# Optimization experiments

Measured on AMD Instinct MI355X. Metric: run time of the kernel, lower is better.

## Reference

```python
import jax, jax.numpy as jnp
import numpy as np
from jax import lax

N_QUBITS = 10
N_LAYERS = 6
DIM = 1 << N_QUBITS
EPS = 1e-5

_i = np.arange(DIM)
# Z_SIGNS[w, i] = (+1/-1) eigenvalue of PauliZ on wire w (wire 0 = most significant bit)
Z_SIGNS = jnp.asarray(np.stack([1.0 - 2.0 * ((_i >> (N_QUBITS - 1 - w)) & 1) for w in range(N_QUBITS)]).astype(np.float32))

def _layer_perm(r):
    # composed permutation of the ring of CNOT(w, (w+r)%n) gates of one StronglyEntanglingLayers layer
    p = _i.copy()
    for w in range(N_QUBITS):
        c, t = w, (w + r) % N_QUBITS
        pc, pt = N_QUBITS - 1 - c, N_QUBITS - 1 - t
        pg = _i ^ (((_i >> pc) & 1) << pt)
        p = p[pg]
    return p

LAYER_PERMS = [jnp.asarray(_layer_perm(l % (N_QUBITS - 1) + 1), dtype=jnp.int32) for l in range(N_LAYERS)]

def _apply_1q(state, U, wire):
    # state: (B, DIM) complex64; U: (2,2) or batched (B,2,2)
    B = state.shape[0]
    left = 1 << wire
    right = DIM // (2 * left)
    s = state.reshape(B, left, 2, right)
    if U.ndim == 3:
        out = jnp.einsum('bij,bljr->blir', U, s)
    else:
        out = jnp.einsum('ij,bljr->blir', U, s)
    return out.reshape(B, DIM)

def _ry_batched(theta):
    c = jnp.cos(theta / 2)
    s = jnp.sin(theta / 2)
    return jnp.stack([jnp.stack([c, -s], -1), jnp.stack([s, c], -1)], -2).astype(jnp.complex64)

def _rot(phi, theta, omega):
    # PennyLane Rot(phi, theta, omega) = RZ(omega) @ RY(theta) @ RZ(phi)
    c = jnp.cos(theta / 2)
    s = jnp.sin(theta / 2)
    m00 = jnp.exp(-1j * (phi + omega) / 2) * c
    m01 = -jnp.exp(1j * (phi - omega) / 2) * s
    m10 = jnp.exp(-1j * (phi - omega) / 2) * s
    m11 = jnp.exp(1j * (phi + omega) / 2) * c
    return jnp.stack([jnp.stack([m00, m01]), jnp.stack([m10, m11])]).astype(jnp.complex64)

def quantum_forward(xq, qw):
    # batched statevector simulation of: RY(pi*x_i) encoding + StronglyEntanglingLayers
    B = xq.shape[0]
    state = jnp.zeros((B, DIM), jnp.complex64).at[:, 0].set(1.0)
    for w in range(N_QUBITS):
        state = _apply_1q(state, _ry_batched(jnp.pi * xq[:, w]), w)
    for l in range(N_LAYERS):
        for w in range(N_QUBITS):
            state = _apply_1q(state, _rot(qw[l, w, 0], qw[l, w, 1], qw[l, w, 2]), w)
        state = state[:, LAYER_PERMS[l]]
    probs = state.real ** 2 + state.imag ** 2
    return probs @ Z_SIGNS.T  # (B, N_QUBITS) expvals of PauliZ

def _conv(x, w, b):
    y = lax.conv_general_dilated(x, w, (1, 1), 'SAME', dimension_numbers=('NCHW', 'OIHW', 'NCHW'))
    return y + b[None, :, None, None]

def _bn(x, g, b):
    # BatchNorm2d in training mode: per-batch statistics over (N, H, W)
    m = jnp.mean(x, (0, 2, 3), keepdims=True)
    v = jnp.var(x, (0, 2, 3), keepdims=True)
    return (x - m) * lax.rsqrt(v + EPS) * g[None, :, None, None] + b[None, :, None, None]

def _pool(x):
    return lax.reduce_window(x, -jnp.inf, lax.max, (1, 1, 2, 2), (1, 1, 2, 2), 'VALID')

def setup_inputs() -> dict:
    key = jax.random.key(0)
    ks = jax.random.split(key, 16)
    n = lambda k, sh, sc: jax.random.normal(k, sh, jnp.float32) * sc
    return {
        'x': jax.random.normal(ks[0], (256, 3, 64, 64), jnp.float32),
        'conv1_w': n(ks[1], (32, 3, 3, 3), 0.1), 'conv1_b': jnp.zeros(32),
        'bn1_g': jnp.ones(32), 'bn1_b': jnp.zeros(32),
        'conv2_w': n(ks[2], (32, 32, 3, 3), 0.05), 'conv2_b': jnp.zeros(32),
        'bn2_g': jnp.ones(32), 'bn2_b': jnp.zeros(32),
        'conv3_w': n(ks[3], (64, 32, 3, 3), 0.05), 'conv3_b': jnp.zeros(64),
        'bn3_g': jnp.ones(64), 'bn3_b': jnp.zeros(64),
        'conv4_w': n(ks[4], (64, 64, 3, 3), 0.05), 'conv4_b': jnp.zeros(64),
        'bn4_g': jnp.ones(64), 'bn4_b': jnp.zeros(64),
        'fc1_w': n(ks[5], (128, 64 * 16 * 16), 0.01), 'fc1_b': jnp.zeros(128),
        'fc2_w': n(ks[6], (10, 128), 0.05), 'fc2_b': jnp.zeros(10),
        'q_weights': jax.random.uniform(ks[7], (6, 10, 3), jnp.float32),
        'head_w': n(ks[8], (10, 10), 0.1), 'head_b': jnp.zeros(10),
    }

def reference(x, conv1_w, conv1_b, bn1_g, bn1_b, conv2_w, conv2_b, bn2_g, bn2_b,
              conv3_w, conv3_b, bn3_g, bn3_b, conv4_w, conv4_b, bn4_g, bn4_b,
              fc1_w, fc1_b, fc2_w, fc2_b, q_weights, head_w, head_b):
    h = jax.nn.relu(_bn(_conv(x, conv1_w, conv1_b), bn1_g, bn1_b))
    h = jax.nn.relu(_bn(_conv(h, conv2_w, conv2_b), bn2_g, bn2_b))
    h = _pool(h)  # Dropout(0.25) is identity in eval
    h = jax.nn.relu(_bn(_conv(h, conv3_w, conv3_b), bn3_g, bn3_b))
    h = jax.nn.relu(_bn(_conv(h, conv4_w, conv4_b), bn4_g, bn4_b))
    h = _pool(h)
    h = h.reshape(h.shape[0], -1)  # (B, 64*16*16)
    h = jax.nn.relu(h @ fc1_w.T + fc1_b)
    h = h @ fc2_w.T + fc2_b  # (B, n_qubits)
    q = quantum_forward(h, q_weights)
    return q @ head_w.T + head_b  # (B, num_classes)
```

## Files before the change

### kernel.cpp

```cpp
#include <hip/hip_runtime.h>
#include <math.h>

#define PI_F 3.14159265358979323846f

typedef __attribute__((ext_vector_type(8))) _Float16 half8;
typedef __attribute__((ext_vector_type(4))) _Float16 half4;
typedef __attribute__((ext_vector_type(4))) float f32x4;

__global__ __launch_bounds__(256) void prep_kernel(
    const float* __restrict__ x, _Float16* __restrict__ X4P,
    const float* __restrict__ w1, const float* __restrict__ w2,
    const float* __restrict__ w3, const float* __restrict__ w4,
    _Float16* __restrict__ t1, _Float16* __restrict__ t2,
    _Float16* __restrict__ t3, _Float16* __restrict__ t4,
    const float* __restrict__ f1w, _Float16* __restrict__ w1t,
    const float* __restrict__ qw, float* __restrict__ rotm,
    unsigned short* __restrict__ perm)
{
    const int b = blockIdx.x;
    const int t = threadIdx.x;
    if (b < 2380) {
        int pp = (b * 256 + t) * 2;
        half8 o;
        #pragma unroll
        for (int j = 0; j < 2; ++j) {
            int p = pp + j;
            int n = p / 4760;
            int rem = p - n * 4760;
            int yp = rem / 68, xp = rem - (rem / 68) * 68;
            int gy = yp - 2, gx = xp - 2;
            float v0 = 0.f, v1 = 0.f, v2 = 0.f;
            if (gy >= 0 && gy < 64 && gx >= 0 && gx < 64) {
                const float* xb = x + (size_t)n * 12288 + gy * 64 + gx;
                v0 = xb[0]; v1 = xb[4096]; v2 = xb[8192];
            }
            o[j * 4 + 0] = (_Float16)v0;
            o[j * 4 + 1] = (_Float16)v1;
            o[j * 4 + 2] = (_Float16)v2;
            o[j * 4 + 3] = (_Float16)0.f;
        }
        *(half8*)&X4P[(size_t)pp * 4] = o;
    } else if (b < 2640) {
        int idx = (b - 2380) * 256 + t;
        if (idx < 9216) {
            int j = idx & 7, co = (idx >> 3) & 31, k8 = idx >> 8;
            int k = k8 * 8 + j, tap = k >> 5, ci = k & 31;
            t2[idx] = (_Float16)w2[(size_t)(co * 32 + ci) * 9 + tap];
        } else if (idx < 27648) {
            int e = idx - 9216;
            int j = e & 7, co = (e >> 3) & 31, r = e >> 8;
            int k8 = r % 36, gg = r / 36;
            int k = k8 * 8 + j, tap = k >> 5, ci = k & 31;
            t3[e] = (_Float16)w3[(size_t)((gg * 32 + co) * 32 + ci) * 9 + tap];
        } else if (idx < 64512) {
            int e = idx - 27648;
            int j = e & 7, co = (e >> 3) & 31, r = e >> 8;
            int k8 = r % 36, gc = r / 36;
            int g = gc >> 1, cc = gc & 1;
            int kl = k8 * 8 + j, tap = kl >> 5, ci = cc * 32 + (kl & 31);
            t4[e] = (_Float16)w4[(size_t)((g * 32 + co) * 64 + ci) * 9 + tap];
        } else if (idx < 66560) {
            int e = idx - 64512;
            int j = e & 7, co = (e >> 3) & 31, k8 = e >> 8;
            int k = k8 * 8 + j, tap = k >> 2, ci = k & 3;
            t1[e] = (_Float16)((tap < 9 && ci < 3) ? w1[(size_t)(co * 3 + ci) * 9 + tap] : 0.f);
        }
    } else if (b < 3152) {
        __shared__ float lds[64][65];
        int b2 = b - 2640;
        const int yx0 = (b2 & 3) * 64;
        const int j = b2 >> 2;
        #pragma unroll
        for (int i = 0; i < 16; ++i) {
            int idx = t + 256 * i;
            int c = idx >> 6, yxl = idx & 63;
            lds[c][yxl] = f1w[(size_t)j * 16384 + c * 256 + yx0 + yxl];
        }
        __syncthreads();
        #pragma unroll
        for (int i = 0; i < 2; ++i) {
            int idx = t + 256 * i;
            int yxl = idx >> 3, c8 = idx & 7;
            half8 h;
            #pragma unroll
            for (int jj = 0; jj < 8; ++jj)
                h[jj] = (_Float16)lds[c8 * 8 + jj][yxl];
            *(half8*)&w1t[(size_t)j * 16384 + (size_t)(yx0 + yxl) * 64 + c8 * 8] = h;
        }
    } else {
        if (t < 60) {
            float phi = qw[t * 3], th = qw[t * 3 + 1], om = qw[t * 3 + 2];
            float c = cosf(0.5f * th), s = sinf(0.5f * th);
            float apo = 0.5f * (phi + om), amo = 0.5f * (phi - om);
            float cpo = cosf(apo), spo = sinf(apo);
            float cmo = cosf(amo), smo = sinf(amo);
            rotm[t * 8 + 0] = cpo * c;  rotm[t * 8 + 1] = -spo * c;
            rotm[t * 8 + 2] = -cmo * s; rotm[t * 8 + 3] = -smo * s;
            rotm[t * 8 + 4] = cmo * s;  rotm[t * 8 + 5] = -smo * s;
            rotm[t * 8 + 6] = cpo * c;  rotm[t * 8 + 7] = spo * c;
        }
        for (int e = t; e < 6144; e += 256) {
            int layer = e >> 10, i = e & 1023;
            int r = layer % 9 + 1;
            int jdx = i;
            for (int w = 9; w >= 0; --w) {
                int tt = (w + r) % 10;
                int pc = 9 - w, pt_ = 9 - tt;
                jdx ^= ((jdx >> pc) & 1) << pt_;
            }
            perm[e] = (unsigned short)jdx;
        }
    }
}

__global__ __launch_bounds__(256) void conv1_stats_kernel(
    const _Float16* __restrict__ X4P, const _Float16* __restrict__ w1m,
    const float* __restrict__ bias, _Float16* __restrict__ Yg,
    float* __restrict__ partials)
{
    constexpr int TC = 66, TR = 6;
    constexpr int NPIX = (TR + 1) * TC;
    __shared__ __align__(16) _Float16 s_in[NPIX * 4];
    __shared__ __align__(16) _Float16 s_w[2048];
    __shared__ __align__(16) _Float16 s_y[256 * 32];
    __shared__ float s_red[64];

    const int t = threadIdx.x;
    const int row0 = blockIdx.x * 4;
    const int n = blockIdx.z;

    *(half8*)&s_w[t * 8] = *(const half8*)&w1m[t * 8];

    for (int p = t; p < NPIX; p += 256) {
        int col = p % TC, r = p / TC;
        uint2 u = make_uint2(0u, 0u);
        if (r < TR) {
            size_t pb = ((size_t)(n * 70 + row0 + r + 1) * 68 + col + 1) * 4;
            u = *(const uint2*)&X4P[pb];
        }
        *(uint2*)&s_in[p * 4] = u;
    }
    if (t < 64) s_red[t] = 0.f;
    __syncthreads();

    const int w = t >> 6, l = t & 63;
    const int lm = l & 15, lg = l >> 4;
    int pA[4];
    #pragma unroll
    for (int f = 0; f < 4; ++f) {
        int m = w * 64 + f * 16 + lm;
        pA[f] = (m >> 6) * TC + (m & 63);
    }
    f32x4 zero4 = {0.f, 0.f, 0.f, 0.f};
    f32x4 acc[4][2];
    #pragma unroll
    for (int f = 0; f < 4; ++f) { acc[f][0] = zero4; acc[f][1] = zero4; }

    {
        const int t0 = lg * 2;
        const int off0 = (t0 / 3) * TC + (t0 % 3);
        const int off1 = ((t0 + 1) / 3) * TC + ((t0 + 1) % 3);
        half8 b0 = *(const half8*)&s_w[(lg * 32 + lm) * 8];
        half8 b1 = *(const half8*)&s_w[(lg * 32 + 16 + lm) * 8];
        #pragma unroll
        for (int f = 0; f < 4; ++f) {
            half4 alo = *(const half4*)&s_in[(pA[f] + off0) * 4];
            half4 ahi = *(const half4*)&s_in[(pA[f] + off1) * 4];
            half8 a;
            #pragma unroll
            for (int j = 0; j < 4; ++j) { a[j] = alo[j]; a[4 + j] = ahi[j]; }
            acc[f][0] = __builtin_amdgcn_mfma_f32_16x16x32_f16(a, b0, acc[f][0], 0, 0, 0);
            acc[f][1] = __builtin_amdgcn_mfma_f32_16x16x32_f16(a, b1, acc[f][1], 0, 0, 0);
        }
    }
    {
        half8 b0 = *(const half8*)&s_w[((4 + lg) * 32 + lm) * 8];
        half8 b1 = *(const half8*)&s_w[((4 + lg) * 32 + 16 + lm) * 8];
        #pragma unroll
        for (int f = 0; f < 4; ++f) {
            half8 a;
            #pragma unroll
            for (int j = 0; j < 8; ++j) a[j] = (_Float16)0.f;
            if (lg == 0) {
                half4 alo = *(const half4*)&s_in[(pA[f] + 134) * 4];
                half4 ahi = *(const half4*)&s_in[(pA[f] + 198) * 4];
                #pragma unroll
                for (int j = 0; j < 4; ++j) { a[j] = alo[j]; a[4 + j] = ahi[j]; }
            }
            acc[f][0] = __builtin_amdgcn_mfma_f32_16x16x32_f16(a, b0, acc[f][0], 0, 0, 0);
            acc[f][1] = __builtin_amdgcn_mfma_f32_16x16x32_f16(a, b1, acc[f][1], 0, 0, 0);
        }
    }

    float bv0 = bias[lm];
    float bv1 = bias[16 + lm];
    float s0 = 0.f, s20 = 0.f, s1 = 0.f, s21 = 0.f;
    #pragma unroll
    for (int f = 0; f < 4; ++f) {
        #pragma unroll
        for (int r = 0; r < 4; ++r) {
            float v0 = acc[f][0][r] + bv0;
            float v1 = acc[f][1][r] + bv1;
            int p_loc = w * 64 + f * 16 + lg * 4 + r;
            s_y[p_loc * 32 + lm] = (_Float16)v0;
            s_y[p_loc * 32 + 16 + lm] = (_Float16)v1;
            s0 += v0; s20 += v0 * v0;
            s1 += v1; s21 += v1 * v1;
        }
    }
    s0 += __shfl_xor(s0, 16);  s0 += __shfl_xor(s0, 32);
    s1 += __shfl_xor(s1, 16);  s1 += __shfl_xor(s1, 32);
    s20 += __shfl_xor(s20, 16); s20 += __shfl_xor(s20, 32);
    s21 += __shfl_xor(s21, 16); s21 += __shfl_xor(s21, 32);
    if (l < 16) {
        atomicAdd(&s_red[lm], s0);
        atomicAdd(&s_red[16 + lm], s1);
        atomicAdd(&s_red[32 + lm], s20);
        atomicAdd(&s_red[48 + lm], s21);
    }
    __syncthreads();

    {
        _Float16* Yb = Yg + ((size_t)(n * 64 + row0) * 64) * 32;
        #pragma unroll
        for (int i = 0; i < 4; ++i) {
            int idx = t + 256 * i;
            *(half8*)&Yb[(size_t)idx * 8] = *(const half8*)&s_y[idx * 8];
        }
    }
    if (t < 64)
        partials[((size_t)n * 16 + blockIdx.x) * 64 + t] = s_red[t];
}

__global__ __launch_bounds__(512, 6) void conv2_fused_kernel(
    const _Float16* __restrict__ Yg, const _Float16* __restrict__ ssh1,
    const _Float16* __restrict__ wt2, const float* __restrict__ c2bias,
    _Float16* __restrict__ out0, _Float16* __restrict__ out1,
    float* __restrict__ partials)
{
    constexpr int COUT = 32, MF = 4, NB = 2;
    constexpr int ROWS = 8;
    constexpr int TC = 66, NPIX = 10 * 66;
    constexpr int PS = 36;
    __shared__ __align__(16) _Float16 s_in[NPIX * PS];
    __shared__ float s_red[64];

    const int t = threadIdx.x;
    const int row0 = blockIdx.x * ROWS;
    const int n = blockIdx.z;
    const int w = t >> 6, l = t & 63;
    const int lm = l & 15, lg = l >> 4;

    if (t < 64) s_red[t] = 0.f;

    {
        const int c8 = t & 3;
        half8 sc = *(const half8*)&ssh1[c8 * 8];
        half8 sh = *(const half8*)&ssh1[32 + c8 * 8];
        for (int idx = t; idx < NPIX * 4; idx += 512) {
            int p = idx >> 2;
            int py = p / 66, px = p - py * 66;
            int gy = row0 - 1 + py, gx = px - 1;
            half8 v;
            #pragma unroll
            for (int j = 0; j < 8; ++j) v[j] = (_Float16)0.f;
            if (gy >= 0 && gy < 64 && gx >= 0 && gx < 64) {
                half8 y = *(const half8*)&Yg[(((size_t)n * 64 + gy) * 64 + gx) * 32 + c8 * 8];
                #pragma unroll
                for (int j = 0; j < 8; ++j) {
                    _Float16 f = y[j] * sc[j] + sh[j];
                    v[j] = f > (_Float16)0.f ? f : (_Float16)0.f;
                }
            }
            half4* vp = (half4*)&v;
            *(half4*)&s_in[p * PS + c8 * 8] = vp[0];
            *(half4*)&s_in[p * PS + c8 * 8 + 4] = vp[1];
        }
    }
    __syncthreads();

    int pA[MF];
    #pragma unroll
    for (int f = 0; f < MF; ++f)
        pA[f] = w * TC + f * 16 + lm;
    f32x4 zero4 = {0.f, 0.f, 0.f, 0.f};
    f32x4 acc[MF][NB];
    #pragma unroll
    for (int f = 0; f < MF; ++f)
        #pragma unroll
        for (int nb = 0; nb < NB; ++nb) acc[f][nb] = zero4;

    #pragma unroll
    for (int tap = 0; tap < 9; ++tap) {
        const int dy = tap / 3, dx = tap % 3;
        const int poff = dy * TC + dx;
        half8 b[NB];
        #pragma unroll
        for (int nb = 0; nb < NB; ++nb) {
            int col = nb * 16 + lm;
            b[nb] = *(const half8*)&wt2[((tap * 4 + lg) * 32 + col) * 8];
        }
        #pragma unroll
        for (int f = 0; f < MF; ++f) {
            int p = pA[f] + poff;
            half4 alo = *(const half4*)&s_in[p * PS + lg * 8];
            half4 ahi = *(const half4*)&s_in[p * PS + lg * 8 + 4];
            half8 a;
            #pragma unroll
            for (int j = 0; j < 4; ++j) { a[j] = alo[j]; a[4 + j] = ahi[j]; }
            #pragma unroll
            for (int nb = 0; nb < NB; ++nb)
                acc[f][nb] = __builtin_amdgcn_mfma_f32_16x16x32_f16(a, b[nb], acc[f][nb], 0, 0, 0);
        }
    }

    float bv[NB], s[NB], s2[NB];
    #pragma unroll
    for (int nb = 0; nb < NB; ++nb) {
        bv[nb] = c2bias[nb * 16 + lm];
        s[nb] = 0.f; s2[nb] = 0.f;
    }
    #pragma unroll
    for (int f = 0; f < MF; ++f) {
        #pragma unroll
        for (int nb = 0; nb < NB; ++nb) {
            #pragma unroll
            for (int r = 0; r < 4; ++r) {
                float v = acc[f][nb][r] + bv[nb];
                acc[f][nb][r] = v;
                s[nb] += v; s2[nb] += v * v;
            }
        }
    }
    #pragma unroll
    for (int nb = 0; nb < NB; ++nb) {
        s[nb] += __shfl_xor(s[nb], 16);  s[nb] += __shfl_xor(s[nb], 32);
        s2[nb] += __shfl_xor(s2[nb], 16); s2[nb] += __shfl_xor(s2[nb], 32);
    }
    if (l < 16) {
        #pragma unroll
        for (int nb = 0; nb < NB; ++nb) {
            atomicAdd(&s_red[nb * 16 + lm], s[nb]);
            atomicAdd(&s_red[32 + nb * 16 + lm], s2[nb]);
        }
    }

    {
        __syncthreads();
        _Float16* pk = s_in;
        #pragma unroll
        for (int nb = 0; nb < NB; ++nb) {
            #pragma unroll
            for (int f = 0; f < MF; ++f) {
                float v0 = acc[f][nb][0], v1 = acc[f][nb][1];
                float v2 = acc[f][nb][2], v3 = acc[f][nb][3];
                int xp0 = f * 8 + lg * 2;
                int o0 = (w * 32 + xp0) * COUT + nb * 16 + lm;
                int o1 = (w * 32 + xp0 + 1) * COUT + nb * 16 + lm;
                pk[o0] = (_Float16)fminf(v0, v1);
                pk[8192 + o0] = (_Float16)fmaxf(v0, v1);
                pk[o1] = (_Float16)fminf(v2, v3);
                pk[8192 + o1] = (_Float16)fmaxf(v2, v3);
            }
        }
        __syncthreads();
        int hp_row = t >> 7, rem = t & 127;
        int xp = rem >> 2, c8 = rem & 3;
        half8 mnA = *(const half8*)&pk[((2 * hp_row) * 32 + xp) * COUT + c8 * 8];
        half8 mnB = *(const half8*)&pk[((2 * hp_row + 1) * 32 + xp) * COUT + c8 * 8];
        half8 mxA = *(const half8*)&pk[8192 + ((2 * hp_row) * 32 + xp) * COUT + c8 * 8];
        half8 mxB = *(const half8*)&pk[8192 + ((2 * hp_row + 1) * 32 + xp) * COUT + c8 * 8];
        half8 mn, mx;
        #pragma unroll
        for (int j = 0; j < 8; ++j) {
            mn[j] = mnA[j] < mnB[j] ? mnA[j] : mnB[j];
            mx[j] = mxA[j] > mxB[j] ? mxA[j] : mxB[j];
        }
        size_t ob = (((size_t)n * 32 + (row0 >> 1) + hp_row) * 32 + xp) * COUT + c8 * 8;
        *(half8*)&out0[ob] = mn;
        *(half8*)&out1[ob] = mx;
    }

    __syncthreads();
    if (t < 64) {
        size_t bid = (size_t)n * gridDim.x + blockIdx.x;
        partials[bid * 64 + t] = s_red[t];
    }
}

template<int BLOCK, int W, int CIN, int COUT, int MF, int NB,
         bool MMIN, bool POOL>
__global__ __launch_bounds__(BLOCK, (BLOCK == 512 ? 4 : 3)) void conv_mfma_kernel(
    const _Float16* __restrict__ in0, const _Float16* __restrict__ in1,
    const _Float16* __restrict__ coef, const _Float16* __restrict__ wt,
    const float* __restrict__ bias,
    _Float16* __restrict__ out0, _Float16* __restrict__ out1,
    float* __restrict__ partials)
{
    constexpr int H = W;
    constexpr int NWAVE = BLOCK / 64;
    constexpr int SPW = MF * 16;
    constexpr int ROWS = NWAVE * SPW / W;
    constexpr int TR = ROWS + 2;
    constexpr int TC = W + 2;
    constexpr int NPIX = TR * TC;
    constexpr int NCH = CIN / 32;
    constexpr int C8N = CIN / 8;
    constexpr int KC = 288;
    constexpr int COUTB = NB * 16;
    __shared__ __align__(16) _Float16 s_in[NPIX * CIN];
    __shared__ float s_red[2 * COUTB];

    const int t = threadIdx.x;
    const int row0 = blockIdx.x * ROWS;
    const int n = blockIdx.z;

    const int w = t >> 6, l = t & 63;
    const int lm = l & 15, lg = l >> 4;
    int pA[MF];
    #pragma unroll
    for (int f = 0; f < MF; ++f) {
        int m = w * SPW + f * 16 + lm;
        pA[f] = (m / W) * TC + (m % W);
    }
    f32x4 zero4 = {0.f, 0.f, 0.f, 0.f};
    f32x4 acc[MF][NB];
    #pragma unroll
    for (int f = 0; f < MF; ++f)
        #pragma unroll
        for (int nb = 0; nb < NB; ++nb) acc[f][nb] = zero4;
    if (t < 2 * COUTB) s_red[t] = 0.f;

    for (int idx = t; idx < NPIX * C8N; idx += BLOCK) {
        int c8 = idx % C8N;
        int p = idx / C8N;
        int col = p % TC, r = p / TC;
        int gy = row0 + r - 1, gx = col - 1;
        half8 v;
        #pragma unroll
        for (int j = 0; j < 8; ++j) v[j] = (_Float16)0.f;
        if (gy >= 0 && gy < H && gx >= 0 && gx < W) {
            size_t gidx = (((size_t)n * H + gy) * W + gx) * CIN + c8 * 8;
            if (MMIN) {
                half8 mn = *(const half8*)&in0[gidx];
                half8 mx = *(const half8*)&in1[gidx];
                half8 sa = *(const half8*)&coef[c8 * 8];
                half8 sb = *(const half8*)&coef[CIN + c8 * 8];
                half8 sh = *(const half8*)&coef[2 * CIN + c8 * 8];
                #pragma unroll
                for (int j = 0; j < 8; ++j) {
                    _Float16 f = mx[j] * sa[j] + mn[j] * sb[j] + sh[j];
                    v[j] = f > (_Float16)0.f ? f : (_Float16)0.f;
                }
            } else {
                v = *(const half8*)&in0[gidx];
                if (coef) {
                    half8 sc = *(const half8*)&coef[c8 * 8];
                    half8 sh = *(const half8*)&coef[CIN + c8 * 8];
                    #pragma unroll
                    for (int j = 0; j < 8; ++j) {
                        _Float16 f = v[j] * sc[j] + sh[j];
                        v[j] = f > (_Float16)0.f ? f : (_Float16)0.f;
                    }
                }
            }
        }
        *(half8*)&s_in[(c8 * NPIX + p) * 8] = v;
    }
    __syncthreads();

    #pragma unroll
    for (int tap = 0; tap < 9; ++tap) {
        const int dy = tap / 3, dx = tap % 3;
        const int poff = dy * TC + dx;
        #pragma unroll
        for (int cc = 0; cc < NCH; ++cc) {
            half8 b[NB];
            #pragma unroll
            for (int nb = 0; nb < NB; ++nb) {
                int cog = nb * 16 + lm;
                int gg = cog >> 5, col = cog & 31;
                const _Float16* wp = wt + (size_t)(gg * NCH + cc) * KC * 32;
                b[nb] = *(const half8*)&wp[((tap * 4 + lg) * 32 + col) * 8];
            }
            #pragma unroll
            for (int f = 0; f < MF; ++f) {
                half8 a = *(const half8*)&s_in[((cc * 4 + lg) * NPIX + pA[f] + poff) * 8];
                #pragma unroll
                for (int nb = 0; nb < NB; ++nb)
                    acc[f][nb] = __builtin_amdgcn_mfma_f32_16x16x32_f16(a, b[nb], acc[f][nb], 0, 0, 0);
            }
        }
    }

    float bv[NB], s[NB], s2[NB];
    #pragma unroll
    for (int nb = 0; nb < NB; ++nb) {
        bv[nb] = bias[nb * 16 + lm];
        s[nb] = 0.f; s2[nb] = 0.f;
    }
    #pragma unroll
    for (int f = 0; f < MF; ++f) {
        #pragma unroll
        for (int r = 0; r < 4; ++r) {
            int m = w * SPW + f * 16 + lg * 4 + r;
            int yy = row0 + m / W, xo = m % W;
            size_t base = (((size_t)n * H + yy) * W + xo) * COUT;
            #pragma unroll
            for (int nb = 0; nb < NB; ++nb) {
                float v = acc[f][nb][r] + bv[nb];
                if (!POOL) out0[base + nb * 16 + lm] = (_Float16)v;
                s[nb] += v; s2[nb] += v * v;
            }
        }
    }
    #pragma unroll
    for (int nb = 0; nb < NB; ++nb) {
        s[nb] += __shfl_xor(s[nb], 16);  s[nb] += __shfl_xor(s[nb], 32);
        s2[nb] += __shfl_xor(s2[nb], 16); s2[nb] += __shfl_xor(s2[nb], 32);
    }
    if (l < 16) {
        #pragma unroll
        for (int nb = 0; nb < NB; ++nb) {
            atomicAdd(&s_red[nb * 16 + lm], s[nb]);
            atomicAdd(&s_red[COUTB + nb * 16 + lm], s2[nb]);
        }
    }

    if (POOL) {
        constexpr int FH = MF / 2;
        constexpr int PPIX = (ROWS / 2) * (W / 2);
        static_assert(2 * PPIX * COUT <= NPIX * CIN, "pool pack fits in s_in");
        __syncthreads();
        _Float16* pk = s_in;
        #pragma unroll
        for (int nb = 0; nb < NB; ++nb) {
            #pragma unroll
            for (int f = 0; f < FH; ++f) {
                #pragma unroll
                for (int rp = 0; rp < 2; ++rp) {
                    float a0 = acc[f][nb][2 * rp] + bv[nb];
                    float a1 = acc[f][nb][2 * rp + 1] + bv[nb];
                    float a2 = acc[f + FH][nb][2 * rp] + bv[nb];
                    float a3 = acc[f + FH][nb][2 * rp + 1] + bv[nb];
                    float mn = fminf(fminf(a0, a1), fminf(a2, a3));
                    float mx = fmaxf(fmaxf(a0, a1), fmaxf(a2, a3));
                    int xp = f * 8 + lg * 2 + rp;
                    int o = (w * (W / 2) + xp) * COUT + nb * 16 + lm;
                    pk[o] = (_Float16)mn;
                    pk[PPIX * COUT + o] = (_Float16)mx;
                }
            }
        }
        __syncthreads();
        size_t gb = (((size_t)n * (H / 2) + (row0 >> 1)) * (W / 2)) * COUT;
        for (int idx = t; idx < PPIX * COUT / 8; idx += BLOCK) {
            *(half8*)&out0[gb + (size_t)idx * 8] = *(const half8*)&pk[idx * 8];
            *(half8*)&out1[gb + (size_t)idx * 8] = *(const half8*)&pk[(PPIX * COUT + idx * 8)];
        }
    }

    __syncthreads();
    if (t < 2 * COUTB) {
        size_t bid = (size_t)n * gridDim.x + blockIdx.x;
        partials[bid * 2 * COUTB + t] = s_red[t];
    }
}

__global__ __launch_bounds__(256) void bn_finalize_kernel(
    const float* __restrict__ partials, int nx, float inv_count,
    const float* __restrict__ gamma, const float* __restrict__ beta,
    float* __restrict__ ss, _Float16* __restrict__ ssh,
    _Float16* __restrict__ sab, int COUT)
{
    const int c = blockIdx.x;
    const int t = threadIdx.x;
    float sum = 0.f, sq = 0.f;
    int total = 256 * nx;
    for (int e = t; e < total; e += 256) {
        size_t off = (size_t)e * 2 * COUT;
        sum += partials[off + c];
        sq  += partials[off + COUT + c];
    }
    #pragma unroll
    for (int off = 32; off > 0; off >>= 1) {
        sum += __shfl_xor(sum, off);
        sq  += __shfl_xor(sq, off);
    }
    __shared__ float rs[4], rq[4];
    if ((t & 63) == 0) { rs[t >> 6] = sum; rq[t >> 6] = sq; }
    __syncthreads();
    if (t == 0) {
        sum = rs[0] + rs[1] + rs[2] + rs[3];
        sq  = rq[0] + rq[1] + rq[2] + rq[3];
        float mean = sum * inv_count;
        float var = sq * inv_count - mean * mean;
        float scale = gamma[c] * rsqrtf(var + 1e-5f);
        float shift = beta[c] - mean * scale;
        ss[c] = scale;
        ss[COUT + c] = shift;
        if (ssh) {
            ssh[c] = (_Float16)scale;
            ssh[COUT + c] = (_Float16)shift;
        }
        if (sab) {
            sab[c] = (_Float16)(scale > 0.f ? scale : 0.f);
            sab[COUT + c] = (_Float16)(scale > 0.f ? 0.f : scale);
            sab[2 * COUT + c] = (_Float16)shift;
        }
    }
}

__global__ __launch_bounds__(256) void fc1_mfma_kernel(
    const _Float16* __restrict__ Amin, const _Float16* __restrict__ Amax,
    const _Float16* __restrict__ sab, const _Float16* __restrict__ Bw,
    float* __restrict__ hp)
{
    __shared__ __align__(16) _Float16 As[64][72];
    __shared__ __align__(16) _Float16 Bs[128][72];
    const int t = threadIdx.x;
    const int mt = blockIdx.x;
    const int kc = blockIdx.y;
    const int w = t >> 6, l = t & 63;
    const int lm = l & 15, lg = l >> 4;

    f32x4 zero4 = {0.f, 0.f, 0.f, 0.f};
    f32x4 acc[8];
    #pragma unroll
    for (int nb = 0; nb < 8; ++nb) acc[nb] = zero4;

    const size_t a_base = (size_t)(mt * 64) * 16384 + (size_t)kc * 512;
    const size_t b_base = (size_t)kc * 512;

    for (int p = 0; p < 8; ++p) {
        __syncthreads();
        #pragma unroll
        for (int i = 0; i < 2; ++i) {
            int idx = t + 256 * i;
            int r = idx >> 3, c8 = idx & 7;
            size_t off = a_base + (size_t)r * 16384 + p * 64 + c8 * 8;
            half8 mn = *(const half8*)&Amin[off];
            half8 mx = *(const half8*)&Amax[off];
            half8 sa = *(const half8*)&sab[c8 * 8];
            half8 sb = *(const half8*)&sab[64 + c8 * 8];
            half8 sh = *(const half8*)&sab[128 + c8 * 8];
            half8 v;
            #pragma unroll
            for (int j = 0; j < 8; ++j) {
                _Float16 f = mx[j] * sa[j] + mn[j] * sb[j] + sh[j];
                v[j] = f > (_Float16)0.f ? f : (_Float16)0.f;
            }
            *(half8*)&As[r][c8 * 8] = v;
        }
        #pragma unroll
        for (int i = 0; i < 4; ++i) {
            int idx = t + 256 * i;
            int r = idx >> 3, c8 = idx & 7;
            *(half8*)&Bs[r][c8 * 8] =
                *(const half8*)&Bw[b_base + (size_t)r * 16384 + p * 64 + c8 * 8];
        }
        __syncthreads();
        #pragma unroll
        for (int ks = 0; ks < 64; ks += 32) {
            half8 a = *(const half8*)&As[w * 16 + lm][ks + lg * 8];
            #pragma unroll
            for (int nb = 0; nb < 8; ++nb) {
                half8 b = *(const half8*)&Bs[nb * 16 + lm][ks + lg * 8];
                acc[nb] = __builtin_amdgcn_mfma_f32_16x16x32_f16(a, b, acc[nb], 0, 0, 0);
            }
        }
    }
    #pragma unroll
    for (int nb = 0; nb < 8; ++nb) {
        #pragma unroll
        for (int r = 0; r < 4; ++r) {
            int row = mt * 64 + w * 16 + lg * 4 + r;
            hp[((size_t)kc * 256 + row) * 128 + nb * 16 + lm] = acc[nb][r];
        }
    }
}

__global__ __launch_bounds__(128) void fcq_kernel(
    const float* __restrict__ hp, const float* __restrict__ f1b,
    const float* __restrict__ f2w, const float* __restrict__ f2b,
    const float* __restrict__ rotm, const unsigned short* __restrict__ perm,
    const float* __restrict__ head_w, const float* __restrict__ head_b,
    float* __restrict__ outp)
{
    __shared__ float lds[2048];
    __shared__ float hl[128];
    __shared__ float xql[10];
    const int n = blockIdx.x;
    const int t = threadIdx.x;

    {
        float s = f1b[t];
        #pragma unroll
        for (int kc = 0; kc < 32; ++kc) s += hp[((size_t)kc * 256 + n) * 128 + t];
        hl[t] = fmaxf(0.f, s);
    }
    __syncthreads();
    if (t < 10) {
        float o = f2b[t];
        #pragma unroll 4
        for (int k = 0; k < 128; ++k) o += f2w[t * 128 + k] * hl[k];
        xql[t] = o;
    }
    __syncthreads();
    if (t >= 64) return;

    const int l = t;
    float ar[16], ai[16];
    #pragma unroll
    for (int r = 0; r < 16; ++r) { ar[r] = 0.f; ai[r] = 0.f; }
    if (l == 0) ar[0] = 1.f;

    #pragma unroll
    for (int w = 0; w < 10; ++w) {
        float th = 0.5f * PI_F * xql[w];
        float c = cosf(th), s = sinf(th);
        const int k = 9 - w;
        if (k >= 6) {
            const int b = k - 6;
            #pragma unroll
            for (int r = 0; r < 16; ++r) {
                if (!(r & (1 << b))) {
                    int r1 = r | (1 << b);
                    float a0 = ar[r], a1 = ar[r1];
                    ar[r]  = c * a0 - s * a1;
                    ar[r1] = s * a0 + c * a1;
                }
            }
        } else {
            float ss = ((l >> k) & 1) ? s : -s;
            #pragma unroll
            for (int r = 0; r < 16; ++r) {
                float p = __shfl_xor(ar[r], 1 << k);
                ar[r] = c * ar[r] + ss * p;
            }
        }
    }

    #pragma unroll 1
    for (int layer = 0; layer < 6; ++layer) {
        #pragma unroll
        for (int w = 0; w < 10; ++w) {
            const float* m = rotm + (layer * 10 + w) * 8;
            float m00r = m[0], m00i = m[1], m01r = m[2], m01i = m[3];
            float m10r = m[4], m10i = m[5], m11r = m[6], m11i = m[7];
            const int k = 9 - w;
            if (k >= 6) {
                const int b = k - 6;
                #pragma unroll
                for (int r = 0; r < 16; ++r) {
                    if (!(r & (1 << b))) {
                        int r1 = r | (1 << b);
                        float a0r = ar[r], a0i = ai[r];
                        float a1r = ar[r1], a1i = ai[r1];
                        ar[r]  = m00r * a0r - m00i * a0i + m01r * a1r - m01i * a1i;
                        ai[r]  = m00r * a0i + m00i * a0r + m01r * a1i + m01i * a1r;
                        ar[r1] = m10r * a0r - m10i * a0i + m11r * a1r - m11i * a1i;
                        ai[r1] = m10r * a0i + m10i * a0r + m11r * a1i + m11i * a1r;
                    }
                }
            } else {
                int bit = (l >> k) & 1;
                float mAr = bit ? m11r : m00r, mAi = bit ? m11i : m00i;
                float mBr = bit ? m10r : m01r, mBi = bit ? m10i : m01i;
                #pragma unroll
                for (int r = 0; r < 16; ++r) {
                    float pr = __shfl_xor(ar[r], 1 << k);
                    float pi = __shfl_xor(ai[r], 1 << k);
                    float mr = ar[r], mi = ai[r];
                    ar[r] = mAr * mr - mAi * mi + mBr * pr - mBi * pi;
                    ai[r] = mAr * mi + mAi * mr + mBr * pi + mBi * pr;
                }
            }
        }
        #pragma unroll
        for (int r = 0; r < 16; ++r) {
            lds[(r << 6) | l] = ar[r];
            lds[1024 + ((r << 6) | l)] = ai[r];
        }
        __syncthreads();
        const unsigned short* pt = perm + layer * 1024;
        #pragma unroll
        for (int r = 0; r < 16; ++r) {
            int ji = pt[(r << 6) | l];
            ar[r] = lds[ji];
            ai[r] = lds[1024 + ji];
        }
        __syncthreads();
    }

    float S = 0.f, T0 = 0.f, T1 = 0.f, T2 = 0.f, T3 = 0.f;
    #pragma unroll
    for (int r = 0; r < 16; ++r) {
        float pr = ar[r] * ar[r] + ai[r] * ai[r];
        S += pr;
        T0 += (r & 1) ? -pr : pr;
        T1 += (r & 2) ? -pr : pr;
        T2 += (r & 4) ? -pr : pr;
        T3 += (r & 8) ? -pr : pr;
    }
    float pk[10];
    pk[0] = T3; pk[1] = T2; pk[2] = T1; pk[3] = T0;
    #pragma unroll
    for (int w = 4; w < 10; ++w)
        pk[w] = ((l >> (9 - w)) & 1) ? -S : S;
    #pragma unroll
    for (int w = 0; w < 10; ++w) {
        #pragma unroll
        for (int off = 1; off < 64; off <<= 1)
            pk[w] += __shfl_xor(pk[w], off);
    }
    if (l < 10) {
        float o = head_b[l];
        #pragma unroll
        for (int kk = 0; kk < 10; ++kk) o += pk[kk] * head_w[l * 10 + kk];
        outp[n * 10 + l] = o;
    }
}

extern "C" void kernel_launch(void* const* d_in, const int* in_sizes, int n_in,
                              void* d_out, int out_size, void* d_ws, size_t ws_size,
                              hipStream_t stream)
{
    const float* x   = (const float*)d_in[0];
    const float* c1w = (const float*)d_in[1];  const float* c1b = (const float*)d_in[2];
    const float* g1  = (const float*)d_in[3];  const float* b1  = (const float*)d_in[4];
    const float* c2w = (const float*)d_in[5];  const float* c2b = (const float*)d_in[6];
    const float* g2  = (const float*)d_in[7];  const float* b2  = (const float*)d_in[8];
    const float* c3w = (const float*)d_in[9];  const float* c3b = (const float*)d_in[10];
    const float* g3  = (const float*)d_in[11]; const float* b3  = (const float*)d_in[12];
    const float* c4w = (const float*)d_in[13]; const float* c4b = (const float*)d_in[14];
    const float* g4  = (const float*)d_in[15]; const float* b4  = (const float*)d_in[16];
    const float* f1w = (const float*)d_in[17]; const float* f1b = (const float*)d_in[18];
    const float* f2w = (const float*)d_in[19]; const float* f2b = (const float*)d_in[20];
    const float* qw  = (const float*)d_in[21];
    const float* hw  = (const float*)d_in[22]; const float* hb  = (const float*)d_in[23];

    float* ws = (float*)d_ws;
    _Float16* H0 = (_Float16*)ws;
    _Float16* H1 = H0 + 33554432;
    float* part = ws + 33554432;
    float* ss1  = part + 524288;
    float* ss2  = ss1 + 64;
    float* ss3  = ss2 + 64;
    float* ss4  = ss3 + 128;
    float* hp   = ss4 + 128;
    float* rotm = hp + 1048576;
    unsigned short* perm16 = (unsigned short*)(rotm + 480);
    _Float16* ssh1 = (_Float16*)(perm16 + 6144);
    _Float16* ssh3 = ssh1 + 64;
    _Float16* sab2 = ssh3 + 128;
    _Float16* sab4 = sab2 + 96;
    _Float16* wt2  = sab4 + 192;
    _Float16* wt3  = wt2 + 9216;
    _Float16* wt4  = wt3 + 18432;
    _Float16* w1m  = wt4 + 36864;
    _Float16* w1t  = w1m + 2048;
    _Float16* X4P  = w1t + 2097152;

    _Float16* Yg    = H0;
    _Float16* minT2 = H1;
    _Float16* maxT2 = H1 + 8388608;
    _Float16* minT4 = H1;
    _Float16* maxT4 = H1 + 4194304;

    prep_kernel<<<3153, 256, 0, stream>>>(x, X4P, c1w, c2w, c3w, c4w,
                                          w1m, wt2, wt3, wt4, f1w, w1t,
                                          qw, rotm, perm16);

    conv1_stats_kernel<<<dim3(16, 1, 256), 256, 0, stream>>>(
        X4P, w1m, c1b, Yg, part);
    bn_finalize_kernel<<<32, 256, 0, stream>>>(part, 16, 1.f / 1048576.f,
                                               g1, b1, ss1, ssh1, nullptr, 32);

    conv2_fused_kernel<<<dim3(8, 1, 256), 512, 0, stream>>>(
        Yg, ssh1, wt2, c2b, minT2, maxT2, part);
    bn_finalize_kernel<<<32, 256, 0, stream>>>(part, 8, 1.f / 1048576.f,
                                               g2, b2, ss2, nullptr, sab2, 32);

    conv_mfma_kernel<512, 32, 32, 64, 4, 4, true, false>
        <<<dim3(2, 1, 256), 512, 0, stream>>>(
        minT2, maxT2, sab2, wt3, c3b, H0, nullptr, part);
    bn_finalize_kernel<<<64, 256, 0, stream>>>(part, 2, 1.f / 262144.f,
                                               g3, b3, ss3, ssh3, nullptr, 64);

    conv_mfma_kernel<512, 32, 64, 64, 4, 4, false, true>
        <<<dim3(2, 1, 256), 512, 0, stream>>>(
        H0, nullptr, ssh3, wt4, c4b, minT4, maxT4, part);
    bn_finalize_kernel<<<64, 256, 0, stream>>>(part, 2, 1.f / 262144.f,
                                               g4, b4, ss4, nullptr, sab4, 64);

    fc1_mfma_kernel<<<dim3(4, 32), 256, 0, stream>>>(minT4, maxT4, sab4, w1t, hp);

    fcq_kernel<<<256, 128, 0, stream>>>(hp, f1b, f2w, f2b,
                                        rotm, perm16, hw, hb, (float*)d_out);
}
```

Measured before the change: 194.9 us.

## Split quantum statevector simulation across four waves with LDS exchange for high qubits

```diff
diff --git a/kernel.cpp b/kernel.cpp
--- a/kernel.cpp
+++ b/kernel.cpp
@@ -680,20 +680,23 @@
     }
 }
 
-__global__ __launch_bounds__(128) void fcq_kernel(
+__global__ __launch_bounds__(256) void fcq_kernel(
     const float* __restrict__ hp, const float* __restrict__ f1b,
     const float* __restrict__ f2w, const float* __restrict__ f2b,
     const float* __restrict__ rotm, const unsigned short* __restrict__ perm,
     const float* __restrict__ head_w, const float* __restrict__ head_b,
     float* __restrict__ outp)
 {
-    __shared__ float lds[2048];
+    __shared__ float lre[1024];
+    __shared__ float lim[1024];
     __shared__ float hl[128];
     __shared__ float xql[10];
     const int n = blockIdx.x;
     const int t = threadIdx.x;
-
-    {
+    const int l = t & 63;
+    const int wv = t >> 6;
+
+    if (t < 128) {
         float s = f1b[t];
         #pragma unroll
         for (int kc = 0; kc < 32; ++kc) s += hp[((size_t)kc * 256 + n) * 128 + t];
@@ -707,23 +710,22 @@
         xql[t] = o;
     }
     __syncthreads();
-    if (t >= 64) return;
-
-    const int l = t;
-    float ar[16], ai[16];
-    #pragma unroll
-    for (int r = 0; r < 16; ++r) { ar[r] = 0.f; ai[r] = 0.f; }
-    if (l == 0) ar[0] = 1.f;
+
+    const int ampb = (wv << 6) | l;
+    float ar[4], ai[4];
+    #pragma unroll
+    for (int r = 0; r < 4; ++r) { ar[r] = 0.f; ai[r] = 0.f; }
+    if (t == 0) ar[0] = 1.f;
 
     #pragma unroll
     for (int w = 0; w < 10; ++w) {
         float th = 0.5f * PI_F * xql[w];
         float c = cosf(th), s = sinf(th);
         const int k = 9 - w;
-        if (k >= 6) {
-            const int b = k - 6;
-            #pragma unroll
-            for (int r = 0; r < 16; ++r) {
+        if (k >= 8) {
+            const int b = k - 8;
+            #pragma unroll
+            for (int r = 0; r < 4; ++r) {
                 if (!(r & (1 << b))) {
                     int r1 = r | (1 << b);
                     float a0 = ar[r], a1 = ar[r1];
@@ -731,10 +733,21 @@
                     ar[r1] = s * a0 + c * a1;
                 }
             }
+        } else if (k >= 6) {
+            #pragma unroll
+            for (int r = 0; r < 4; ++r) lre[(r << 8) | ampb] = ar[r];
+            __syncthreads();
+            float ss = ((wv >> (k - 6)) & 1) ? s : -s;
+            #pragma unroll
+            for (int r = 0; r < 4; ++r) {
+                float p = lre[((r << 8) | ampb) ^ (1 << k)];
+                ar[r] = c * ar[r] + ss * p;
+            }
+            __syncthreads();
         } else {
             float ss = ((l >> k) & 1) ? s : -s;
             #pragma unroll
-            for (int r = 0; r < 16; ++r) {
+            for (int r = 0; r < 4; ++r) {
                 float p = __shfl_xor(ar[r], 1 << k);
                 ar[r] = c * ar[r] + ss * p;
             }
@@ -749,10 +762,10 @@
             float m00r = m[0], m00i = m[1], m01r = m[2], m01i = m[3];
             float m10r = m[4], m10i = m[5], m11r = m[6], m11i = m[7];
             const int k = 9 - w;
-            if (k >= 6) {
-                const int b = k - 6;
+            if (k >= 8) {
+                const int b = k - 8;
                 #pragma unroll
-                for (int r = 0; r < 16; ++r) {
+                for (int r = 0; r < 4; ++r) {
                     if (!(r & (1 << b))) {
                         int r1 = r | (1 << b);
                         float a0r = ar[r], a0i = ai[r];
@@ -763,12 +776,31 @@
                         ai[r1] = m10r * a0i + m10i * a0r + m11r * a1i + m11i * a1r;
                     }
                 }
+            } else if (k >= 6) {
+                #pragma unroll
+                for (int r = 0; r < 4; ++r) {
+                    lre[(r << 8) | ampb] = ar[r];
+                    lim[(r << 8) | ampb] = ai[r];
+                }
+                __syncthreads();
+                int bit = (wv >> (k - 6)) & 1;
+                float mAr = bit ? m11r : m00r, mAi = bit ? m11i : m00i;
+                float mBr = bit ? m10r : m01r, mBi = bit ? m10i : m01i;
+                #pragma unroll
+                for (int r = 0; r < 4; ++r) {
+                    int pa = ((r << 8) | ampb) ^ (1 << k);
+                    float pr = lre[pa], pi = lim[pa];
+                    float mr = ar[r], mi = ai[r];
+                    ar[r] = mAr * mr - mAi * mi + mBr * pr - mBi * pi;
+                    ai[r] = mAr * mi + mAi * mr + mBr * pi + mBi * pr;
+                }
+                __syncthreads();
             } else {
                 int bit = (l >> k) & 1;
                 float mAr = bit ? m11r : m00r, mAi = bit ? m11i : m00i;
                 float mBr = bit ? m10r : m01r, mBi = bit ? m10i : m01i;
                 #pragma unroll
-                for (int r = 0; r < 16; ++r) {
+                for (int r = 0; r < 4; ++r) {
                     float pr = __shfl_xor(ar[r], 1 << k);
                     float pi = __shfl_xor(ai[r], 1 << k);
                     float mr = ar[r], mi = ai[r];
@@ -778,33 +810,34 @@
             }
         }
         #pragma unroll
-        for (int r = 0; r < 16; ++r) {
-            lds[(r << 6) | l] = ar[r];
-            lds[1024 + ((r << 6) | l)] = ai[r];
+        for (int r = 0; r < 4; ++r) {
+            lre[(r << 8) | ampb] = ar[r];
+            lim[(r << 8) | ampb] = ai[r];
         }
         __syncthreads();
         const unsigned short* pt = perm + layer * 1024;
         #pragma unroll
-        for (int r = 0; r < 16; ++r) {
-            int ji = pt[(r << 6) | l];
-            ar[r] = lds[ji];
-            ai[r] = lds[1024 + ji];
+        for (int r = 0; r < 4; ++r) {
+            int ji = pt[(r << 8) | ampb];
+            ar[r] = lre[ji];
+            ai[r] = lim[ji];
         }
         __syncthreads();
     }
 
-    float S = 0.f, T0 = 0.f, T1 = 0.f, T2 = 0.f, T3 = 0.f;
-    #pragma unroll
-    for (int r = 0; r < 16; ++r) {
+    float S = 0.f, T9 = 0.f, T8 = 0.f;
+    #pragma unroll
+    for (int r = 0; r < 4; ++r) {
         float pr = ar[r] * ar[r] + ai[r] * ai[r];
         S += pr;
-        T0 += (r & 1) ? -pr : pr;
-        T1 += (r & 2) ? -pr : pr;
-        T2 += (r & 4) ? -pr : pr;
-        T3 += (r & 8) ? -pr : pr;
+        T9 += (r & 2) ? -pr : pr;
+        T8 += (r & 1) ? -pr : pr;
     }
     float pk[10];
-    pk[0] = T3; pk[1] = T2; pk[2] = T1; pk[3] = T0;
+    pk[0] = T9;
+    pk[1] = T8;
+    pk[2] = ((wv >> 1) & 1) ? -S : S;
+    pk[3] = (wv & 1) ? -S : S;
     #pragma unroll
     for (int w = 4; w < 10; ++w)
         pk[w] = ((l >> (9 - w)) & 1) ? -S : S;
@@ -814,11 +847,21 @@
         for (int off = 1; off < 64; off <<= 1)
             pk[w] += __shfl_xor(pk[w], off);
     }
-    if (l < 10) {
-        float o = head_b[l];
-        #pragma unroll
-        for (int kk = 0; kk < 10; ++kk) o += pk[kk] * head_w[l * 10 + kk];
-        outp[n * 10 + l] = o;
+    if (l == 0) {
+        #pragma unroll
+        for (int w = 0; w < 10; ++w) lre[wv * 16 + w] = pk[w];
+    }
+    __syncthreads();
+    if (t < 10) {
+        float tot = lre[t] + lre[16 + t] + lre[32 + t] + lre[48 + t];
+        lre[64 + t] = tot;
+    }
+    __syncthreads();
+    if (t < 10) {
+        float o = head_b[t];
+        #pragma unroll
+        for (int kk = 0; kk < 10; ++kk) o += lre[64 + kk] * head_w[t * 10 + kk];
+        outp[n * 10 + t] = o;
     }
 }
 
@@ -896,6 +939,6 @@
 
     fc1_mfma_kernel<<<dim3(4, 32), 256, 0, stream>>>(minT4, maxT4, sab4, w1t, hp);
 
-    fcq_kernel<<<256, 128, 0, stream>>>(hp, f1b, f2w, f2b,
+    fcq_kernel<<<256, 256, 0, stream>>>(hp, f1b, f2w, f2b,
                                         rotm, perm16, hw, hb, (float*)d_out);
 }
```

Result: faster. 184.4 us (-5.4%).
